# Optimization experiments

Hardware: AMD Instinct MI355X
Metric: run time of the kernel (lower is better)

The kernel has to match this reference:

```python
import jax, jax.numpy as jnp
import numpy as np
from jax import lax

B = 64          # batch
IMG = 384       # image H=W
PATCH = 16      # stem patch size -> 24x24 grid
C = 192         # hidden_channels
K = 5           # knn_graph k (hard-coded in extract_graph)
HG = IMG // PATCH
N = HG * HG     # total_num_nodes = 576
HID = 4 * C     # FFN expansion
PRED_HID = 1024
NUM_CLASSES = 1


def setup_inputs() -> dict:
    key = jax.random.key(0)
    ks = jax.random.split(key, 16)
    def w(k, shape, s=0.02):
        return jax.random.normal(k, shape, jnp.float32) * s
    f32 = jnp.float32
    return {
        "x": jax.random.normal(ks[0], (B, 3, IMG, IMG), f32),
        # stem: 16x16 patch-embed conv
        "stem_w": w(ks[1], (C, 3, PATCH, PATCH)),
        "stem_b": jnp.zeros((C,), f32),
        "pos_embed": w(ks[2], (1, C, HG, HG)),
        # GSAT edge-attention MLP: concat(src,dst) -> C -> 1 -> sigmoid
        "att_w1": w(ks[3], (2 * C, C)), "att_b1": jnp.zeros((C,), f32),
        "att_w2": w(ks[4], (C, 1)),     "att_b2": jnp.zeros((1,), f32),
        # two message-passing layers (GIN-style update)
        "gnn_w1": w(ks[5], (C, C)), "gnn_b1": jnp.zeros((C,), f32),
        "gnn_w2": w(ks[6], (C, C)), "gnn_b2": jnp.zeros((C,), f32),
        # FFN (1x1 convs == channel matmuls), BN in eval mode (mean0/var1)
        "ffn_w1": w(ks[7], (C, HID)), "ffn_b1": jnp.zeros((HID,), f32),
        "ffn_g1": jnp.ones((HID,), f32), "ffn_be1": jnp.zeros((HID,), f32),
        "ffn_w2": w(ks[8], (HID, C)), "ffn_b2": jnp.zeros((C,), f32),
        "ffn_g2": jnp.ones((C,), f32), "ffn_be2": jnp.zeros((C,), f32),
        # prediction head: 1x1 conv C->1024, BN(eval), gelu, 1x1 conv 1024->num_classes
        "pred_w1": w(ks[9], (C, PRED_HID)), "pred_b1": jnp.zeros((PRED_HID,), f32),
        "pred_g": jnp.ones((PRED_HID,), f32), "pred_be": jnp.zeros((PRED_HID,), f32),
        "pred_w2": w(ks[10], (PRED_HID, NUM_CLASSES)), "pred_b2": jnp.zeros((NUM_CLASSES,), f32),
    }


def reference(x, stem_w, stem_b, pos_embed,
              att_w1, att_b1, att_w2, att_b2,
              gnn_w1, gnn_b1, gnn_w2, gnn_b2,
              ffn_w1, ffn_b1, ffn_g1, ffn_be1,
              ffn_w2, ffn_b2, ffn_g2, ffn_be2,
              pred_w1, pred_b1, pred_g, pred_be, pred_w2, pred_b2):
    # ---- stem + pos_embed ----
    feat = lax.conv_general_dilated(x, stem_w, (PATCH, PATCH), 'VALID',
                                    dimension_numbers=('NCHW', 'OIHW', 'NCHW'))
    feat = feat + stem_b[None, :, None, None] + pos_embed        # [B,C,Hg,Wg]
    b, c, hg, wg = feat.shape
    n = hg * wg
    nf = feat.reshape(b, c, n).transpose(0, 2, 1)                # [B,N,C]
    nfd = lax.stop_gradient(nf)                                  # extract_graph under no_grad

    # ---- kNN graph build: per-image pairwise sq. distances + top-k ----
    sq = jnp.sum(nfd * nfd, axis=-1)                             # [B,N]
    d2 = sq[:, :, None] + sq[:, None, :] - 2.0 * jnp.einsum('bnc,bmc->bnm', nfd, nfd)
    d2 = d2 + jnp.eye(n, dtype=d2.dtype) * 1e9                   # exclude self-loops
    _, idx = lax.top_k(-d2, K)                                   # [B,N,K] nearest neighbors
    src = (idx + (jnp.arange(b) * n)[:, None, None]).reshape(-1)  # [E] global neighbor idx
    dst = jnp.repeat(jnp.arange(b * n), K)                        # [E] global center idx

    # ---- GSAT GNN: edge attention + attention-weighted message passing ----
    h = nfd.reshape(b * n, c)                                    # [BN,C] (detached)
    e = jax.nn.relu(jnp.concatenate([h[src], h[dst]], axis=-1) @ att_w1 + att_b1)
    edge_att = jax.nn.sigmoid(e @ att_w2 + att_b2)               # [E,1]
    for Wg, bg in ((gnn_w1, gnn_b1), (gnn_w2, gnn_b2)):
        m = jax.ops.segment_sum(edge_att * h[src], dst, num_segments=b * n)
        h = jax.nn.relu((h + m) @ Wg + bg)                       # GIN-style update

    # ---- FFN (1x1 convs) with residual, BN eval-mode affine ----
    t = h.reshape(b, n, c)                                       # [B,N,C]
    u = jax.nn.gelu((t @ ffn_w1 + ffn_b1) * ffn_g1 + ffn_be1, approximate=False)
    t = t + ((u @ ffn_w2 + ffn_b2) * ffn_g2 + ffn_be2)

    # ---- global average pool + prediction head ----
    g = jnp.mean(t, axis=1)                                      # [B,C]
    p = jax.nn.gelu((g @ pred_w1 + pred_b1) * pred_g + pred_be, approximate=False)
    prediction = p @ pred_w2 + pred_b2                           # [B,num_classes]
    return edge_att, prediction
```

## Files before the change

### kernel.cpp

```cpp
#include <hip/hip_runtime.h>
#include <hip/hip_bf16.h>
#include <math.h>

constexpr int B_    = 64;
constexpr int C_    = 192;
constexpr int N_    = 576;
constexpr int BN_   = B_ * N_;
constexpr int K_    = 5;
constexpr int E_    = BN_ * K_;

__device__ __forceinline__ float gelu_exact(float x) {
    return 0.5f * x * (1.0f + erff(x * 0.70710678118654752440f));
}

__device__ __forceinline__ float bf2f(unsigned short v) {
    return __uint_as_float(((unsigned)v) << 16);
}
__device__ __forceinline__ unsigned short f2bf(float x) {
    __hip_bfloat16 h = __float2bfloat16(x);
    return *(unsigned short*)&h;
}

__global__ __launch_bounds__(256) void transpose_w_k(const float* __restrict__ w,
                                                     float* __restrict__ wt) {
    int gid = blockIdx.x * 256 + threadIdx.x;
    int k = gid / 192, oc = gid % 192;
    wt[gid] = w[oc * 768 + k];
}

__global__ __launch_bounds__(256) void stem_gemm96_k(
    const float* __restrict__ x, const float* __restrict__ Wt,
    const float* __restrict__ sb, const float* __restrict__ pos,
    float* __restrict__ nf)
{
    __shared__ float As[96][68];
    __shared__ float Ws[64][68];
    const int tid = threadIdx.x;
    const int tr = tid >> 4, tc = tid & 15;
    const int mb = blockIdx.x;
    const int nb = blockIdx.y;
    const int b  = mb / 6;
    const int n0 = (mb % 6) * 96;

    float4 acc[6];
    #pragma unroll
    for (int i = 0; i < 6; ++i) acc[i] = float4{0.f, 0.f, 0.f, 0.f};

    for (int kc = 0; kc < 768; kc += 64) {
        #pragma unroll
        for (int i = 0; i < 6; ++i) {
            int q = i * 256 + tid;
            int m = q >> 4, kq = q & 15;
            int k = kc + kq * 4;
            int ci = k >> 8, rem = k & 255, dy = rem >> 4, dx = rem & 15;
            int n = n0 + m, py = n / 24, px = n % 24;
            const float* src = &x[(((size_t)(b * 3 + ci) * 384) + py * 16 + dy) * 384
                                  + px * 16 + dx];
            *(float4*)&As[m][kq * 4] = *(const float4*)src;
        }
        #pragma unroll
        for (int i = 0; i < 4; ++i) {
            int q = i * 256 + tid;
            int m = q >> 4, kq = q & 15;
            *(float4*)&Ws[m][kq * 4] =
                *(const float4*)&Wt[(size_t)(kc + m) * 192 + nb * 64 + kq * 4];
        }
        __syncthreads();
        #pragma unroll
        for (int k4 = 0; k4 < 64; k4 += 4) {
            float4 a4[6], b4[4];
            #pragma unroll
            for (int i = 0; i < 6; ++i) a4[i] = *(const float4*)&As[tr * 6 + i][k4];
            #pragma unroll
            for (int kk = 0; kk < 4; ++kk) b4[kk] = *(const float4*)&Ws[k4 + kk][tc * 4];
            #pragma unroll
            for (int i = 0; i < 6; ++i) {
                const float av[4] = {a4[i].x, a4[i].y, a4[i].z, a4[i].w};
                #pragma unroll
                for (int kk = 0; kk < 4; ++kk) {
                    acc[i].x += av[kk] * b4[kk].x;
                    acc[i].y += av[kk] * b4[kk].y;
                    acc[i].z += av[kk] * b4[kk].z;
                    acc[i].w += av[kk] * b4[kk].w;
                }
            }
        }
        __syncthreads();
    }

    #pragma unroll
    for (int i = 0; i < 6; ++i) {
        int n = n0 + tr * 6 + i;
        int row = b * 576 + n;
        int oc0 = nb * 64 + tc * 4;
        float v[4] = {acc[i].x, acc[i].y, acc[i].z, acc[i].w};
        #pragma unroll
        for (int j = 0; j < 4; ++j) {
            int oc = oc0 + j;
            v[j] = v[j] + sb[oc] + pos[oc * 576 + n];
        }
        *(float4*)&nf[(size_t)row * 192 + oc0] = float4{v[0], v[1], v[2], v[3]};
    }
}

__global__ __launch_bounds__(256) void sq_k(const float* __restrict__ nf,
                                            float* __restrict__ sq) {
    int wid = threadIdx.x >> 6, lane = threadIdx.x & 63;
    int n = blockIdx.x * 4 + wid;
    const float* row = nf + (size_t)n * 192;
    float s = 0.f;
    #pragma unroll
    for (int c = 0; c < 3; ++c) { float v = row[lane + c * 64]; s += v * v; }
    #pragma unroll
    for (int off = 32; off; off >>= 1) s += __shfl_down(s, off);
    if (lane == 0) sq[n] = s;
}

__global__ void transpose_nf_k(const float* __restrict__ nf, float* __restrict__ nfT) {
    __shared__ float tile[32][33];
    int b = blockIdx.z;
    int n0 = blockIdx.x * 32, c0 = blockIdx.y * 32;
    int tx = threadIdx.x, ty = threadIdx.y;
    #pragma unroll
    for (int r = 0; r < 4; ++r) {
        int i = ty * 4 + r;
        tile[i][tx] = nf[((size_t)b * 576 + n0 + i) * 192 + c0 + tx];
    }
    __syncthreads();
    #pragma unroll
    for (int r = 0; r < 4; ++r) {
        int i = ty * 4 + r;
        nfT[((size_t)b * 192 + c0 + i) * 576 + n0 + tx] = tile[tx][i];
    }
}

__global__ __launch_bounds__(64) void knn_sym_k(
    const float* __restrict__ nfT, const float* __restrict__ sqn,
    float* __restrict__ candV, int* __restrict__ candI)
{
    __shared__ float smem[64 * 69];
    float* As  = smem;
    float* Bs  = smem + 2048;
    float* d2s = smem;

    const int tid = threadIdx.x;
    const int tr = tid >> 3, tc = tid & 7;
    const int b = blockIdx.y;
    int t = blockIdx.x;
    int bi = 0;
    while (t >= 9 - bi) { t -= 9 - bi; ++bi; }
    const int bj = bi + t;
    const int r0 = bi * 64, c0 = bj * 64;

    float acc[8][8];
    #pragma unroll
    for (int i = 0; i < 8; ++i)
        #pragma unroll
        for (int j = 0; j < 8; ++j) acc[i][j] = 0.f;

    for (int kc = 0; kc < 192; kc += 32) {
        #pragma unroll
        for (int i = 0; i < 8; ++i) {
            int q = i * 64 + tid;
            int k = q >> 4, c4 = (q & 15) * 4;
            const float* srow = &nfT[((size_t)(b * 192 + kc + k)) * 576];
            *(float4*)&As[k * 64 + c4] = *(const float4*)&srow[r0 + c4];
            *(float4*)&Bs[k * 64 + c4] = *(const float4*)&srow[c0 + c4];
        }
        __syncthreads();
        #pragma unroll 8
        for (int kk = 0; kk < 32; ++kk) {
            float4 a0 = *(const float4*)&As[kk * 64 + tr * 8];
            float4 a1 = *(const float4*)&As[kk * 64 + tr * 8 + 4];
            float4 b0 = *(const float4*)&Bs[kk * 64 + tc * 8];
            float4 b1 = *(const float4*)&Bs[kk * 64 + tc * 8 + 4];
            const float av[8] = {a0.x, a0.y, a0.z, a0.w, a1.x, a1.y, a1.z, a1.w};
            const float bv[8] = {b0.x, b0.y, b0.z, b0.w, b1.x, b1.y, b1.z, b1.w};
            #pragma unroll
            for (int i = 0; i < 8; ++i)
                #pragma unroll
                for (int j = 0; j < 8; ++j)
                    acc[i][j] += av[i] * bv[j];
        }
        __syncthreads();
    }

    #pragma unroll
    for (int i = 0; i < 8; ++i) {
        int rl = tr * 8 + i, rg = r0 + rl;
        float sr = sqn[b * 576 + rg];
        #pragma unroll
        for (int j = 0; j < 8; ++j) {
            int cl = tc * 8 + j, cg = c0 + cl;
            float d = sr + sqn[b * 576 + cg] - 2.f * acc[i][j];
            if (cg == rg) d += 1e9f;
            d2s[rl * 69 + cl] = d;
        }
    }
    __syncthreads();

    {
        const int r = tid;
        float tv[5]; int ti[5];
        #pragma unroll
        for (int p = 0; p < 5; ++p) { tv[p] = 3.4e38f; ti[p] = 0; }
        for (int c = 0; c < 64; ++c) {
            float cv = d2s[r * 69 + c];
            if (cv < tv[4]) {
                int ci = c0 + c;
                #pragma unroll
                for (int q = 0; q < 5; ++q) {
                    bool less = cv < tv[q];
                    float nv = less ? tv[q] : cv;
                    int ni   = less ? ti[q] : ci;
                    tv[q] = less ? cv : tv[q];
                    ti[q] = less ? ci : ti[q];
                    cv = nv; ci = ni;
                }
            }
        }
        int gr = b * 576 + r0 + r;
        #pragma unroll
        for (int p = 0; p < 5; ++p) {
            candV[(size_t)gr * 45 + bj * 5 + p] = tv[p];
            candI[(size_t)gr * 45 + bj * 5 + p] = ti[p];
        }
    }

    if (bi != bj) {
        const int c = tid;
        float tv[5]; int ti[5];
        #pragma unroll
        for (int p = 0; p < 5; ++p) { tv[p] = 3.4e38f; ti[p] = 0; }
        for (int r = 0; r < 64; ++r) {
            float cv = d2s[r * 69 + c];
            if (cv < tv[4]) {
                int ci = r0 + r;
                #pragma unroll
                for (int q = 0; q < 5; ++q) {
                    bool less = cv < tv[q];
                    float nv = less ? tv[q] : cv;
                    int ni   = less ? ti[q] : ci;
                    tv[q] = less ? cv : tv[q];
                    ti[q] = less ? ci : ti[q];
                    cv = nv; ci = ni;
                }
            }
        }
        int gr = b * 576 + c0 + c;
        #pragma unroll
        for (int p = 0; p < 5; ++p) {
            candV[(size_t)gr * 45 + bi * 5 + p] = tv[p];
            candI[(size_t)gr * 45 + bi * 5 + p] = tv[p] == tv[p] ? ti[p] : ti[p];
        }
        #pragma unroll
        for (int p = 0; p < 5; ++p) {
            candI[(size_t)gr * 45 + bi * 5 + p] = ti[p];
        }
    }
}

__global__ __launch_bounds__(256) void knn_merge_k(
    const float* __restrict__ candV, const int* __restrict__ candI,
    int* __restrict__ idxOut)
{
    int r = blockIdx.x * 256 + threadIdx.x;
    float tv[5]; int ti[5];
    #pragma unroll
    for (int p = 0; p < 5; ++p) { tv[p] = 3.4e38f; ti[p] = 0; }
    #pragma unroll 5
    for (int s = 0; s < 45; ++s) {
        float cv = candV[(size_t)r * 45 + s];
        if (cv < tv[4]) {
            int cidx = candI[(size_t)r * 45 + s];
            #pragma unroll
            for (int q = 0; q < 5; ++q) {
                bool less = cv < tv[q];
                float nv = less ? tv[q] : cv;
                int ni   = less ? ti[q] : cidx;
                tv[q] = less ? cv : tv[q];
                ti[q] = less ? cidx : ti[q];
                cv = nv; cidx = ni;
            }
        }
    }
    int base = (r / 576) * 576;
    #pragma unroll
    for (int p = 0; p < 5; ++p) idxOut[r * 5 + p] = base + ti[p];
}

template <int EPI>
__global__ __launch_bounds__(256) void gemm_rm_k(
    const float* __restrict__ A, const float* __restrict__ W, float* __restrict__ out,
    int M, int N, int K,
    const float* __restrict__ bias, const float* __restrict__ gsc,
    const float* __restrict__ gsh, const float* __restrict__ res)
{
    __shared__ float As[64][68];
    __shared__ float Ws[64][68];
    const int tid = threadIdx.x;
    const int tr = tid >> 4, tc = tid & 15;
    const int mBase = blockIdx.x * 64, nBase = blockIdx.y * 64;

    float4 acc[4];
    acc[0] = acc[1] = acc[2] = acc[3] = float4{0.f, 0.f, 0.f, 0.f};

    for (int kc = 0; kc < K; kc += 64) {
        #pragma unroll
        for (int i = 0; i < 4; ++i) {
            int q = i * 256 + tid;
            int m = q >> 4, kq = q & 15;
            *(float4*)&As[m][kq * 4] =
                *(const float4*)&A[(size_t)(mBase + m) * K + kc + kq * 4];
            *(float4*)&Ws[m][kq * 4] =
                *(const float4*)&W[(size_t)(kc + m) * N + nBase + kq * 4];
        }
        __syncthreads();
        #pragma unroll
        for (int k4 = 0; k4 < 64; k4 += 4) {
            float4 a4[4], b4[4];
            #pragma unroll
            for (int i = 0; i < 4; ++i) a4[i] = *(const float4*)&As[tr * 4 + i][k4];
            #pragma unroll
            for (int kk = 0; kk < 4; ++kk) b4[kk] = *(const float4*)&Ws[k4 + kk][tc * 4];
            #pragma unroll
            for (int i = 0; i < 4; ++i) {
                const float av[4] = {a4[i].x, a4[i].y, a4[i].z, a4[i].w};
                #pragma unroll
                for (int kk = 0; kk < 4; ++kk) {
                    acc[i].x += av[kk] * b4[kk].x;
                    acc[i].y += av[kk] * b4[kk].y;
                    acc[i].z += av[kk] * b4[kk].z;
                    acc[i].w += av[kk] * b4[kk].w;
                }
            }
        }
        __syncthreads();
    }

    #pragma unroll
    for (int i = 0; i < 4; ++i) {
        int row = mBase + tr * 4 + i;
        int n0 = nBase + tc * 4;
        float v[4] = {acc[i].x, acc[i].y, acc[i].z, acc[i].w};
        #pragma unroll
        for (int j = 0; j < 4; ++j) {
            int n = n0 + j;
            float xv = v[j];
            if (EPI == 1) xv += bias[n];
            if (EPI == 2) { xv += bias[n]; xv = fmaxf(xv, 0.f); }
            if (EPI == 3) { xv = (xv + bias[n]) * gsc[n] + gsh[n]; xv = gelu_exact(xv); }
            if (EPI == 4) {
                xv = res[(size_t)row * N + n] + (xv + bias[n]) * gsc[n] + gsh[n];
            }
            v[j] = xv;
        }
        *(float4*)&out[(size_t)row * N + n0] = float4{v[0], v[1], v[2], v[3]};
    }
}

template <int EPI>
__global__ __launch_bounds__(256) void gemm_mfma_k(
    const unsigned short* __restrict__ A, const unsigned short* __restrict__ Bt,
    unsigned short* __restrict__ out, int M, int N, int K,
    const float* __restrict__ bias, const float* __restrict__ gsc,
    const float* __restrict__ gsh, const unsigned short* __restrict__ res)
{
    using frag = __attribute__((ext_vector_type(8))) short;
    using facc = __attribute__((ext_vector_type(4))) float;
    __shared__ unsigned short As[256][72];
    __shared__ unsigned short Bs[64][72];
    const int tid = threadIdx.x;
    const int wave = tid >> 6, lane = tid & 63;
    const int m16 = lane & 15, quad = lane >> 4;
    const int mBase = blockIdx.x * 256, nBase = blockIdx.y * 64;

    facc zero = {0.f, 0.f, 0.f, 0.f};
    facc acc[4][4];
    #pragma unroll
    for (int ms = 0; ms < 4; ++ms)
        #pragma unroll
        for (int t = 0; t < 4; ++t) acc[ms][t] = zero;

    for (int kc = 0; kc < K; kc += 64) {
        #pragma unroll
        for (int r = 0; r < 8; ++r) {
            int q = r * 256 + tid;
            int row = q >> 3, c8 = (q & 7) * 8;
            *(int4*)&As[row][c8] =
                *(const int4*)&A[(size_t)(mBase + row) * K + kc + c8];
        }
        #pragma unroll
        for (int r = 0; r < 2; ++r) {
            int q = r * 256 + tid;
            int row = q >> 3, c8 = (q & 7) * 8;
            *(int4*)&Bs[row][c8] =
                *(const int4*)&Bt[(size_t)(nBase + row) * K + kc + c8];
        }
        __syncthreads();
        #pragma unroll
        for (int kk = 0; kk < 64; kk += 32) {
            frag bfr[4];
            #pragma unroll
            for (int t = 0; t < 4; ++t)
                bfr[t] = *(const frag*)&Bs[t * 16 + m16][kk + quad * 8];
            #pragma unroll
            for (int ms = 0; ms < 4; ++ms) {
                frag a = *(const frag*)&As[64 * wave + ms * 16 + m16][kk + quad * 8];
                #pragma unroll
                for (int t = 0; t < 4; ++t)
                    acc[ms][t] = __builtin_amdgcn_mfma_f32_16x16x32_bf16(a, bfr[t], acc[ms][t], 0, 0, 0);
            }
        }
        __syncthreads();
    }

    #pragma unroll
    for (int ms = 0; ms < 4; ++ms) {
        #pragma unroll
        for (int t = 0; t < 4; ++t) {
            #pragma unroll
            for (int r = 0; r < 4; ++r) {
                int row = mBase + 64 * wave + ms * 16 + quad * 4 + r;
                int col = nBase + t * 16 + m16;
                float xv = acc[ms][t][r];
                if (EPI == 2) { xv += bias[col]; xv = fmaxf(xv, 0.f); }
                if (EPI == 3) { xv = (xv + bias[col]) * gsc[col] + gsh[col]; xv = gelu_exact(xv); }
                if (EPI == 4) {
                    xv = bf2f(res[(size_t)row * N + col]) + (xv + bias[col]) * gsc[col] + gsh[col];
                }
                out[(size_t)row * N + col] = f2bf(xv);
            }
        }
    }
}

template <int EPI>
__global__ __launch_bounds__(256) void gemm_mfma_split_k(
    const unsigned short* __restrict__ Ah, const unsigned short* __restrict__ Al,
    const unsigned short* __restrict__ Bh, const unsigned short* __restrict__ Bl,
    float* __restrict__ out, int M, int N, int K, const float* __restrict__ bias)
{
    using frag = __attribute__((ext_vector_type(8))) short;
    using facc = __attribute__((ext_vector_type(4))) float;
    __shared__ unsigned short AsH[64][72], AsL[64][72];
    __shared__ unsigned short BsH[64][72], BsL[64][72];
    const int tid = threadIdx.x;
    const int wave = tid >> 6, lane = tid & 63;
    const int m16 = lane & 15, quad = lane >> 4;
    const int mBase = blockIdx.x * 64, nBase = blockIdx.y * 64;

    facc zero = {0.f, 0.f, 0.f, 0.f};
    facc acc[4];
    #pragma unroll
    for (int t = 0; t < 4; ++t) acc[t] = zero;

    for (int kc = 0; kc < K; kc += 64) {
        #pragma unroll
        for (int r = 0; r < 2; ++r) {
            int q = r * 256 + tid;
            int row = q >> 3, c8 = (q & 7) * 8;
            *(int4*)&AsH[row][c8] = *(const int4*)&Ah[(size_t)(mBase + row) * K + kc + c8];
            *(int4*)&AsL[row][c8] = *(const int4*)&Al[(size_t)(mBase + row) * K + kc + c8];
            *(int4*)&BsH[row][c8] = *(const int4*)&Bh[(size_t)(nBase + row) * K + kc + c8];
            *(int4*)&BsL[row][c8] = *(const int4*)&Bl[(size_t)(nBase + row) * K + kc + c8];
        }
        __syncthreads();
        #pragma unroll
        for (int kk = 0; kk < 64; kk += 32) {
            frag ah = *(const frag*)&AsH[16 * wave + m16][kk + quad * 8];
            frag al = *(const frag*)&AsL[16 * wave + m16][kk + quad * 8];
            #pragma unroll
            for (int t = 0; t < 4; ++t) {
                frag bh = *(const frag*)&BsH[t * 16 + m16][kk + quad * 8];
                frag bl = *(const frag*)&BsL[t * 16 + m16][kk + quad * 8];
                acc[t] = __builtin_amdgcn_mfma_f32_16x16x32_bf16(ah, bh, acc[t], 0, 0, 0);
                acc[t] = __builtin_amdgcn_mfma_f32_16x16x32_bf16(ah, bl, acc[t], 0, 0, 0);
                acc[t] = __builtin_amdgcn_mfma_f32_16x16x32_bf16(al, bh, acc[t], 0, 0, 0);
            }
        }
        __syncthreads();
    }

    #pragma unroll
    for (int t = 0; t < 4; ++t) {
        #pragma unroll
        for (int r = 0; r < 4; ++r) {
            int row = mBase + 16 * wave + quad * 4 + r;
            int col = nBase + t * 16 + m16;
            float xv = acc[t][r];
            if (EPI == 1) xv += bias[col];
            out[(size_t)row * N + col] = xv;
        }
    }
}

__global__ __launch_bounds__(256) void asplit_k(const float* __restrict__ a,
                                                unsigned short* __restrict__ hi,
                                                unsigned short* __restrict__ lo) {
    int g = blockIdx.x * 256 + threadIdx.x;
    float v = a[g];
    unsigned short h = f2bf(v);
    hi[g] = h;
    lo[g] = f2bf(v - bf2f(h));
}

__global__ __launch_bounds__(256) void wsplit_att_k(const float* __restrict__ w,
                                                    unsigned short* __restrict__ hi,
                                                    unsigned short* __restrict__ lo) {
    int gid = blockIdx.x * 256 + threadIdx.x;
    int half = gid / 36864, r = gid % 36864;
    int n = r / 192, k = r % 192;
    float v = w[(size_t)(half * 192 + k) * 192 + n];
    unsigned short h = f2bf(v);
    hi[gid] = h;
    lo[gid] = f2bf(v - bf2f(h));
}

__global__ __launch_bounds__(256) void wprep_k(const float* __restrict__ w,
                                               unsigned short* __restrict__ wt,
                                               int K, int N) {
    int gid = blockIdx.x * 256 + threadIdx.x;
    int n = gid / K, k = gid % K;
    wt[gid] = f2bf(w[(size_t)k * N + n]);
}

__global__ __launch_bounds__(256) void edge_att_k(
    const float* __restrict__ hA, const float* __restrict__ hB,
    const int* __restrict__ idx, const float* __restrict__ w2,
    const float* __restrict__ b2, float* __restrict__ att)
{
    int wid = threadIdx.x >> 6, lane = threadIdx.x & 63;
    int e = blockIdx.x * 4 + wid;
    int dst = e / K_;
    int src = idx[e];
    float s = 0.f;
    #pragma unroll
    for (int c0 = 0; c0 < 3; ++c0) {
        int c = lane + c0 * 64;
        float v = hA[(size_t)src * 192 + c] + hB[(size_t)dst * 192 + c];
        v = fmaxf(v, 0.f);
        s += v * w2[c];
    }
    #pragma unroll
    for (int off = 32; off; off >>= 1) s += __shfl_down(s, off);
    if (lane == 0) att[e] = 1.f / (1.f + expf(-(s + b2[0])));
}

__device__ __forceinline__ float ldv(const float* p, size_t i) { return p[i]; }
__device__ __forceinline__ float ldv(const unsigned short* p, size_t i) { return bf2f(p[i]); }

template <typename TI>
__global__ __launch_bounds__(256) void msg_bf_k(
    const TI* __restrict__ h, const float* __restrict__ att,
    const int* __restrict__ idx, unsigned short* __restrict__ s)
{
    int g = blockIdx.x * 256 + threadIdx.x;
    int n = g / 192, c = g % 192;
    float acc = ldv(h, (size_t)g);
    #pragma unroll
    for (int p = 0; p < K_; ++p) {
        int sp = idx[n * K_ + p];
        acc += att[n * K_ + p] * ldv(h, (size_t)sp * 192 + c);
    }
    s[g] = f2bf(acc);
}

__global__ void pool_bf16_k(const unsigned short* __restrict__ t, float* __restrict__ g) {
    int b = blockIdx.x, c = threadIdx.x;
    float s = 0.f;
    for (int n = 0; n < 576; ++n) s += bf2f(t[((size_t)b * 576 + n) * 192 + c]);
    g[b * 192 + c] = s * (1.f / 576.f);
}

__global__ __launch_bounds__(256) void head2_k(
    const float* __restrict__ p, const float* __restrict__ w2,
    const float* __restrict__ b2, float* __restrict__ out)
{
    int b = blockIdx.x;
    float s = 0.f;
    for (int j = threadIdx.x; j < 1024; j += 256) s += p[(size_t)b * 1024 + j] * w2[j];
    #pragma unroll
    for (int off = 32; off; off >>= 1) s += __shfl_down(s, off);
    __shared__ float ls[4];
    int wid = threadIdx.x >> 6, lane = threadIdx.x & 63;
    if (lane == 0) ls[wid] = s;
    __syncthreads();
    if (threadIdx.x == 0) out[b] = ls[0] + ls[1] + ls[2] + ls[3] + b2[0];
}

extern "C" void kernel_launch(void* const* d_in, const int* in_sizes, int n_in,
                              void* d_out, int out_size, void* d_ws, size_t ws_size,
                              hipStream_t stream) {
    const float* x        = (const float*)d_in[0];
    const float* stem_w   = (const float*)d_in[1];
    const float* stem_b   = (const float*)d_in[2];
    const float* pos      = (const float*)d_in[3];
    const float* att_w1   = (const float*)d_in[4];
    const float* att_b1   = (const float*)d_in[5];
    const float* att_w2   = (const float*)d_in[6];
    const float* att_b2   = (const float*)d_in[7];
    const float* gnn_w1   = (const float*)d_in[8];
    const float* gnn_b1   = (const float*)d_in[9];
    const float* gnn_w2   = (const float*)d_in[10];
    const float* gnn_b2   = (const float*)d_in[11];
    const float* ffn_w1   = (const float*)d_in[12];
    const float* ffn_b1   = (const float*)d_in[13];
    const float* ffn_g1   = (const float*)d_in[14];
    const float* ffn_be1  = (const float*)d_in[15];
    const float* ffn_w2   = (const float*)d_in[16];
    const float* ffn_b2   = (const float*)d_in[17];
    const float* ffn_g2   = (const float*)d_in[18];
    const float* ffn_be2  = (const float*)d_in[19];
    const float* pred_w1  = (const float*)d_in[20];
    const float* pred_b1  = (const float*)d_in[21];
    const float* pred_g   = (const float*)d_in[22];
    const float* pred_be  = (const float*)d_in[23];
    const float* pred_w2  = (const float*)d_in[24];
    const float* pred_b2  = (const float*)d_in[25];

    float* ws = (float*)d_ws;
    const size_t RSZ = (size_t)BN_ * C_;
    float* R0 = ws;
    float* R1 = R0 + RSZ;
    float* R2 = R1 + RSZ;
    float* R3 = R2 + RSZ;
    float* sqb = R3 + RSZ;
    int*   idxb = (int*)(sqb + BN_);
    float* gb = (float*)(idxb + E_);
    float* pb = gb + 64 * C_;
    unsigned short* wg1T = (unsigned short*)(pb + 64 * 1024);
    unsigned short* wg2T = wg1T + 192 * 192;
    unsigned short* wf1T = wg2T + 192 * 192;
    unsigned short* wf2T = wf1T + 768 * 192;
    unsigned short* waHi = wf2T + 192 * 768;
    unsigned short* waLo = waHi + 2 * 192 * 192;

    float* candV = R1;
    int*   candI = (int*)(R1 + (size_t)BN_ * 45);

    unsigned short* Sb    = (unsigned short*)R1;
    unsigned short* Hb    = (unsigned short*)(R1 + RSZ / 2);
    unsigned short* Tb    = (unsigned short*)R2;
    unsigned short* ToutB = (unsigned short*)(R2 + RSZ / 2);
    unsigned short* Ahi   = (unsigned short*)R3;
    unsigned short* Alo   = Ahi + RSZ;
    unsigned short* Ub    = (unsigned short*)R3;

    float* att  = (float*)d_out;
    float* pred = att + E_;

    float* Wt = R3;

    wprep_k<<<144, 256, 0, stream>>>(gnn_w1, wg1T, 192, 192);
    wprep_k<<<144, 256, 0, stream>>>(gnn_w2, wg2T, 192, 192);
    wprep_k<<<576, 256, 0, stream>>>(ffn_w1, wf1T, 192, 768);
    wprep_k<<<576, 256, 0, stream>>>(ffn_w2, wf2T, 768, 192);
    wsplit_att_k<<<288, 256, 0, stream>>>(att_w1, waHi, waLo);

    transpose_w_k<<<576, 256, 0, stream>>>(stem_w, Wt);
    stem_gemm96_k<<<dim3(384, 3), 256, 0, stream>>>(x, Wt, stem_b, pos, R0);

    sq_k<<<BN_ / 4, 256, 0, stream>>>(R0, sqb);
    transpose_nf_k<<<dim3(18, 6, 64), dim3(32, 8), 0, stream>>>(R0, R3);
    knn_sym_k<<<dim3(45, 64), 64, 0, stream>>>(R3, sqb, candV, candI);
    knn_merge_k<<<BN_ / 256, 256, 0, stream>>>(candV, candI, idxb);

    asplit_k<<<BN_ * C_ / 256, 256, 0, stream>>>(R0, Ahi, Alo);
    gemm_mfma_split_k<0><<<dim3(576, 3), 256, 0, stream>>>(Ahi, Alo,
        waHi, waLo, R1, BN_, 192, 192, nullptr);
    gemm_mfma_split_k<1><<<dim3(576, 3), 256, 0, stream>>>(Ahi, Alo,
        waHi + 36864, waLo + 36864, R2, BN_, 192, 192, att_b1);
    edge_att_k<<<E_ / 4, 256, 0, stream>>>(R1, R2, idxb, att_w2, att_b2, att);

    msg_bf_k<float><<<BN_ * C_ / 256, 256, 0, stream>>>(R0, att, idxb, Sb);
    gemm_mfma_k<2><<<dim3(144, 3), 256, 0, stream>>>(Sb, wg1T, Hb,
        BN_, 192, 192, gnn_b1, nullptr, nullptr, nullptr);
    msg_bf_k<unsigned short><<<BN_ * C_ / 256, 256, 0, stream>>>(Hb, att, idxb, Sb);
    gemm_mfma_k<2><<<dim3(144, 3), 256, 0, stream>>>(Sb, wg2T, Tb,
        BN_, 192, 192, gnn_b2, nullptr, nullptr, nullptr);

    for (int ch = 0; ch < 2; ++ch) {
        const unsigned short* Ain = Tb + (size_t)ch * 18432 * 192;
        unsigned short* Tout = ToutB + (size_t)ch * 18432 * 192;
        gemm_mfma_k<3><<<dim3(72, 12), 256, 0, stream>>>(Ain, wf1T, Ub,
            18432, 768, 192, ffn_b1, ffn_g1, ffn_be1, nullptr);
        gemm_mfma_k<4><<<dim3(72, 3), 256, 0, stream>>>(Ub, wf2T, Tout,
            18432, 192, 768, ffn_b2, ffn_g2, ffn_be2, Ain);
    }

    pool_bf16_k<<<64, 192, 0, stream>>>(ToutB, gb);
    gemm_rm_k<3><<<dim3(1, 16), 256, 0, stream>>>(gb, pred_w1, pb,
        64, 1024, 192, pred_b1, pred_g, pred_be, nullptr);
    head2_k<<<64, 256, 0, stream>>>(pb, pred_w2, pred_b2, pred);
}
```

Measured before the change: 773.6 us.

## Retile stem GEMM to full-width output tiles with register-prefetched loads

The stem patch-embed GEMM now computes a 64-row by 192-column tile per block instead of 96x64, with a 32-wide K step. Because every block covers all output channels, each image patch element is gathered from x once rather than three times. Global loads for the next K chunk are prefetched into registers while the current chunk is computed, which adds register pressure (48 accumulators per thread) and removes the explicit launch bounds. A redundant duplicate store loop in the kNN candidate write is also removed.

```diff
diff --git a/kernel.cpp b/kernel.cpp
--- a/kernel.cpp
+++ b/kernel.cpp
@@ -28,60 +28,85 @@
     wt[gid] = w[oc * 768 + k];
 }
 
-__global__ __launch_bounds__(256) void stem_gemm96_k(
+__global__ void stem_gemm64w_k(
     const float* __restrict__ x, const float* __restrict__ Wt,
     const float* __restrict__ sb, const float* __restrict__ pos,
     float* __restrict__ nf)
 {
-    __shared__ float As[96][68];
-    __shared__ float Ws[64][68];
+    __shared__ float As[64][36];
+    __shared__ float Ws[32][200];
     const int tid = threadIdx.x;
     const int tr = tid >> 4, tc = tid & 15;
     const int mb = blockIdx.x;
-    const int nb = blockIdx.y;
-    const int b  = mb / 6;
-    const int n0 = (mb % 6) * 96;
-
-    float4 acc[6];
-    #pragma unroll
-    for (int i = 0; i < 6; ++i) acc[i] = float4{0.f, 0.f, 0.f, 0.f};
-
-    for (int kc = 0; kc < 768; kc += 64) {
-        #pragma unroll
-        for (int i = 0; i < 6; ++i) {
+    const int b  = mb / 9;
+    const int n0 = (mb % 9) * 64;
+
+    float4 acc[4][3];
+    #pragma unroll
+    for (int i = 0; i < 4; ++i)
+        #pragma unroll
+        for (int g = 0; g < 3; ++g) acc[i][g] = float4{0.f, 0.f, 0.f, 0.f};
+
+    float4 aP[2], wP[6];
+    auto gatherA = [&](int kc) {
+        #pragma unroll
+        for (int i = 0; i < 2; ++i) {
             int q = i * 256 + tid;
-            int m = q >> 4, kq = q & 15;
+            int m = q >> 3, kq = q & 7;
             int k = kc + kq * 4;
             int ci = k >> 8, rem = k & 255, dy = rem >> 4, dx = rem & 15;
             int n = n0 + m, py = n / 24, px = n % 24;
-            const float* src = &x[(((size_t)(b * 3 + ci) * 384) + py * 16 + dy) * 384
-                                  + px * 16 + dx];
-            *(float4*)&As[m][kq * 4] = *(const float4*)src;
-        }
-        #pragma unroll
-        for (int i = 0; i < 4; ++i) {
+            aP[i] = *(const float4*)&x[(((size_t)(b * 3 + ci) * 384) + py * 16 + dy) * 384
+                                       + px * 16 + dx];
+        }
+    };
+    auto loadW = [&](int kc) {
+        #pragma unroll
+        for (int i = 0; i < 6; ++i) {
             int q = i * 256 + tid;
-            int m = q >> 4, kq = q & 15;
-            *(float4*)&Ws[m][kq * 4] =
-                *(const float4*)&Wt[(size_t)(kc + m) * 192 + nb * 64 + kq * 4];
-        }
-        __syncthreads();
-        #pragma unroll
-        for (int k4 = 0; k4 < 64; k4 += 4) {
-            float4 a4[6], b4[4];
-            #pragma unroll
-            for (int i = 0; i < 6; ++i) a4[i] = *(const float4*)&As[tr * 6 + i][k4];
-            #pragma unroll
-            for (int kk = 0; kk < 4; ++kk) b4[kk] = *(const float4*)&Ws[k4 + kk][tc * 4];
-            #pragma unroll
-            for (int i = 0; i < 6; ++i) {
-                const float av[4] = {a4[i].x, a4[i].y, a4[i].z, a4[i].w};
+            int wr = q / 48, c4 = (q % 48) * 4;
+            wP[i] = *(const float4*)&Wt[(size_t)(kc + wr) * 192 + c4];
+        }
+    };
+
+    gatherA(0); loadW(0);
+    for (int kc = 0; kc < 768; kc += 32) {
+        #pragma unroll
+        for (int i = 0; i < 2; ++i) {
+            int q = i * 256 + tid;
+            int m = q >> 3, kq = q & 7;
+            *(float4*)&As[m][kq * 4] = aP[i];
+        }
+        #pragma unroll
+        for (int i = 0; i < 6; ++i) {
+            int q = i * 256 + tid;
+            int wr = q / 48, c4 = (q % 48) * 4;
+            *(float4*)&Ws[wr][c4] = wP[i];
+        }
+        __syncthreads();
+        if (kc + 32 < 768) { gatherA(kc + 32); loadW(kc + 32); }
+        #pragma unroll
+        for (int k4 = 0; k4 < 32; k4 += 4) {
+            float4 a4[4];
+            #pragma unroll
+            for (int i = 0; i < 4; ++i) a4[i] = *(const float4*)&As[tr + i * 16][k4];
+            #pragma unroll
+            for (int kk = 0; kk < 4; ++kk) {
+                float4 b4[3];
                 #pragma unroll
-                for (int kk = 0; kk < 4; ++kk) {
-                    acc[i].x += av[kk] * b4[kk].x;
-                    acc[i].y += av[kk] * b4[kk].y;
-                    acc[i].z += av[kk] * b4[kk].z;
-                    acc[i].w += av[kk] * b4[kk].w;
+                for (int g = 0; g < 3; ++g)
+                    b4[g] = *(const float4*)&Ws[k4 + kk][tc * 12 + g * 4];
+                #pragma unroll
+                for (int i = 0; i < 4; ++i) {
+                    const float av = (kk == 0) ? a4[i].x : (kk == 1) ? a4[i].y
+                                   : (kk == 2) ? a4[i].z : a4[i].w;
+                    #pragma unroll
+                    for (int g = 0; g < 3; ++g) {
+                        acc[i][g].x += av * b4[g].x;
+                        acc[i][g].y += av * b4[g].y;
+                        acc[i][g].z += av * b4[g].z;
+                        acc[i][g].w += av * b4[g].w;
+                    }
                 }
             }
         }
@@ -89,17 +114,20 @@
     }
 
     #pragma unroll
-    for (int i = 0; i < 6; ++i) {
-        int n = n0 + tr * 6 + i;
+    for (int i = 0; i < 4; ++i) {
+        int n = n0 + tr + i * 16;
         int row = b * 576 + n;
-        int oc0 = nb * 64 + tc * 4;
-        float v[4] = {acc[i].x, acc[i].y, acc[i].z, acc[i].w};
-        #pragma unroll
-        for (int j = 0; j < 4; ++j) {
-            int oc = oc0 + j;
-            v[j] = v[j] + sb[oc] + pos[oc * 576 + n];
-        }
-        *(float4*)&nf[(size_t)row * 192 + oc0] = float4{v[0], v[1], v[2], v[3]};
+        #pragma unroll
+        for (int g = 0; g < 3; ++g) {
+            int oc0 = tc * 12 + g * 4;
+            float v[4] = {acc[i][g].x, acc[i][g].y, acc[i][g].z, acc[i][g].w};
+            #pragma unroll
+            for (int j = 0; j < 4; ++j) {
+                int oc = oc0 + j;
+                v[j] = v[j] + sb[oc] + pos[oc * 576 + n];
+            }
+            *(float4*)&nf[(size_t)row * 192 + oc0] = float4{v[0], v[1], v[2], v[3]};
+        }
     }
 }
 
@@ -251,10 +279,6 @@
         #pragma unroll
         for (int p = 0; p < 5; ++p) {
             candV[(size_t)gr * 45 + bi * 5 + p] = tv[p];
-            candI[(size_t)gr * 45 + bi * 5 + p] = tv[p] == tv[p] ? ti[p] : ti[p];
-        }
-        #pragma unroll
-        for (int p = 0; p < 5; ++p) {
             candI[(size_t)gr * 45 + bi * 5 + p] = ti[p];
         }
     }
@@ -659,7 +683,7 @@
     wsplit_att_k<<<288, 256, 0, stream>>>(att_w1, waHi, waLo);
 
     transpose_w_k<<<576, 256, 0, stream>>>(stem_w, Wt);
-    stem_gemm96_k<<<dim3(384, 3), 256, 0, stream>>>(x, Wt, stem_b, pos, R0);
+    stem_gemm64w_k<<<576, 256, 0, stream>>>(x, Wt, stem_b, pos, R0);
 
     sq_k<<<BN_ / 4, 256, 0, stream>>>(R0, sqb);
     transpose_nf_k<<<dim3(18, 6, 64), dim3(32, 8), 0, stream>>>(R0, R3);
```

After: 1.043 ms. 34.8% more time.
